# Kernel optimization log

Measured on AMD Instinct MI355X. Metric: run time of the kernel, lower is better.

## Reference

```python
import jax, jax.numpy as jnp
import numpy as np

N = 2048          # n_nodes
D = 512           # d_model
H = 8             # n_heads
DH = D // H       # head dim
FF = 4 * D
MAX_DIST = 10
LN_EPS = 1e-5


def setup_inputs() -> dict:
    key = jax.random.key(0)
    ks = jax.random.split(key, 20)
    s = 1.0 / np.sqrt(D)
    sf = 1.0 / np.sqrt(FF)
    return {
        "x": jax.random.normal(ks[0], (N, D), jnp.float32),
        "adj": (jax.random.uniform(ks[1], (N, N)) < 0.01).astype(jnp.float32),
        "spatial_emb": jax.random.normal(ks[2], (MAX_DIST + 1,), jnp.float32) * 0.02,
        "wq": jax.random.normal(ks[3], (D, D), jnp.float32) * s,
        "bq": jnp.zeros((D,), jnp.float32),
        "wk": jax.random.normal(ks[4], (D, D), jnp.float32) * s,
        "bk": jnp.zeros((D,), jnp.float32),
        "wv": jax.random.normal(ks[5], (D, D), jnp.float32) * s,
        "bv": jnp.zeros((D,), jnp.float32),
        "wo": jax.random.normal(ks[6], (D, D), jnp.float32) * s,
        "bo": jnp.zeros((D,), jnp.float32),
        "ln1_w": jnp.ones((D,), jnp.float32),
        "ln1_b": jnp.zeros((D,), jnp.float32),
        "w1": jax.random.normal(ks[7], (FF, D), jnp.float32) * s,
        "b1": jnp.zeros((FF,), jnp.float32),
        "w2": jax.random.normal(ks[8], (D, FF), jnp.float32) * sf,
        "b2": jnp.zeros((D,), jnp.float32),
        "ln2_w": jnp.ones((D,), jnp.float32),
        "ln2_b": jnp.zeros((D,), jnp.float32),
    }


def floyd_warshall(adj):
    # dist init: 1 where edge, inf otherwise, 0 on diagonal
    n = adj.shape[0]
    dist = jnp.where(adj > 0, 1.0, jnp.inf)
    dist = jnp.where(jnp.eye(n, dtype=bool), 0.0, dist)

    def body(k, dmat):
        row = jax.lax.dynamic_slice_in_dim(dmat, k, 1, axis=0)  # [1, n]
        col = jax.lax.dynamic_slice_in_dim(dmat, k, 1, axis=1)  # [n, 1]
        return jnp.minimum(dmat, col + row)

    dist = jax.lax.fori_loop(0, n, body, dist)
    return jnp.clip(dist, 0, MAX_DIST).astype(jnp.int32)  # [n, n]


def layer_norm(x, w, b):
    mu = jnp.mean(x, axis=-1, keepdims=True)
    var = jnp.mean(jnp.square(x - mu), axis=-1, keepdims=True)
    return (x - mu) * jax.lax.rsqrt(var + LN_EPS) * w + b


def reference(x, adj, spatial_emb, wq, bq, wk, bk, wv, bv, wo, bo,
              ln1_w, ln1_b, w1, b1, w2, b2, ln2_w, ln2_b):
    n = x.shape[0]
    sp_dist = floyd_warshall(adj)                       # [n, n] int32 in [0, 10]
    bias = spatial_emb[sp_dist]                         # [n, n] additive attn bias

    # multi-head attention with additive spatial bias (shared across heads)
    q = (x @ wq.T + bq).reshape(n, H, DH).transpose(1, 0, 2)  # [h, n, dh]
    k = (x @ wk.T + bk).reshape(n, H, DH).transpose(1, 0, 2)
    v = (x @ wv.T + bv).reshape(n, H, DH).transpose(1, 0, 2)
    scores = jnp.einsum('hnd,hmd->hnm', q, k) / np.sqrt(DH) + bias[None]
    attn = jax.nn.softmax(scores, axis=-1)
    ctx = jnp.einsum('hnm,hmd->hnd', attn, v)           # [h, n, dh]
    attn_out = ctx.transpose(1, 0, 2).reshape(n, D) @ wo.T + bo

    h = layer_norm(x + attn_out, ln1_w, ln1_b)
    ffn = jax.nn.gelu(h @ w1.T + b1, approximate=False) @ w2.T + b2
    return layer_norm(h + ffn, ln2_w, ln2_b)
```

## Files before the change

kernel.cpp:

```cpp
#include <hip/hip_runtime.h>
#include <cstdint>
#include <cstddef>


typedef __attribute__((ext_vector_type(8))) short short8;
typedef __attribute__((ext_vector_type(4))) float f32x4;

#define N_NODES 2048
#define DMODEL  512
#define NHEAD   8
#define DHEAD   64
#define FFDIM   2048

#define OFF_ADJB   (0)
#define OFF_DIST   (0x80000)
#define OFF_XB     (0x480000)
#define OFF_WQB    (0x680000)
#define OFF_WKB    (0x700000)
#define OFF_WVB    (0x780000)
#define OFF_WOB    (0x800000)
#define OFF_W1B    (0x880000)
#define OFF_W2B    (0xA80000)
#define OFF_QM     (0xC80000)
#define OFF_KM     (0xE80000)
#define OFF_VT     (0x1080000)
#define OFF_CTX    (0x1280000)
#define OFF_ATMP   (0x1480000)
#define OFF_H1     (0x1880000)
#define OFF_H1B    (0x1C80000)
#define OFF_MID    (0x1E80000)
#define OFF_FFN2   (0x2680000)

__device__ __forceinline__ unsigned short f2bf(float f) {
  union { float f; unsigned u; } c; c.f = f;
  unsigned r = c.u + 0x7FFFu + ((c.u >> 16) & 1u);
  return (unsigned short)(r >> 16);
}

__device__ __forceinline__ float bf2f(unsigned short u) {
  union { unsigned u; float f; } c; c.u = ((unsigned)u) << 16;
  return c.f;
}

__device__ __forceinline__ uint32_t cvtpk_bf16(float lo, float hi) {
  uint32_t r;
  asm("v_cvt_pk_bf16_f32 %0, %1, %2" : "=v"(r) : "v"(lo), "v"(hi));
  return r;
}

typedef const __attribute__((address_space(1))) unsigned int* as1_u32p;
typedef __attribute__((address_space(3))) unsigned int* as3_u32p;
__device__ __forceinline__ void gload_lds16(const void* g, void* l) {
  __builtin_amdgcn_global_load_lds((as1_u32p)g, (as3_u32p)l, 16, 0, 0);
}

__global__ void cvt_all_kernel(const float* __restrict__ x,
                               const float* __restrict__ wq, const float* __restrict__ wk,
                               const float* __restrict__ wv, const float* __restrict__ wo,
                               const float* __restrict__ w1, const float* __restrict__ w2,
                               unsigned short* __restrict__ xb,
                               unsigned short* __restrict__ wqb, unsigned short* __restrict__ wkb,
                               unsigned short* __restrict__ wvb, unsigned short* __restrict__ wob,
                               unsigned short* __restrict__ w1b, unsigned short* __restrict__ w2b) {
  int i = blockIdx.x * 256 + threadIdx.x;
  const float* src; unsigned short* dst; int off;
  if (i < 262144)      { src = x;  dst = xb;  off = i; }
  else if (i < 327680) { src = wq; dst = wqb; off = i - 262144; }
  else if (i < 393216) { src = wk; dst = wkb; off = i - 327680; }
  else if (i < 458752) { src = wv; dst = wvb; off = i - 393216; }
  else if (i < 524288) { src = wo; dst = wob; off = i - 458752; }
  else if (i < 786432) { src = w1; dst = w1b; off = i - 524288; }
  else                 { src = w2; dst = w2b; off = i - 786432; }
  float4 v = ((const float4*)src)[off];
  unsigned p0 = (unsigned)f2bf(v.x) | ((unsigned)f2bf(v.y) << 16);
  unsigned p1 = (unsigned)f2bf(v.z) | ((unsigned)f2bf(v.w) << 16);
  ((uint2*)dst)[off] = make_uint2(p0, p1);
}

__global__ void pack_adj_kernel(const float* __restrict__ adj, uint32_t* __restrict__ adjb) {
  int i = blockIdx.x;
  int tid = threadIdx.x, wid = tid >> 6, lane = tid & 63;
  for (int it = 0; it < 8; ++it) {
    int jbase = it * 256 + wid * 64;
    int j = jbase + lane;
    unsigned long long m = __ballot(adj[(size_t)i * 2048 + j] > 0.0f);
    int w32 = jbase >> 5;
    if (lane == 0)  adjb[i * 64 + w32]     = (uint32_t)m;
    if (lane == 32) adjb[i * 64 + w32 + 1] = (uint32_t)(m >> 32);
  }
}

__device__ __forceinline__ void bfs_body(int i, const uint32_t* __restrict__ adjb,
                                         uint8_t* __restrict__ dist, char* smem) {
  int tid = threadIdx.x, wid = tid >> 6, lane = tid & 63;

  uint4* comb_v = (uint4*)smem;
  uint32_t* wtot = (uint32_t*)(smem + 4096);
  uint16_t* list_s = (uint16_t*)(smem + 4112);
  const uint32_t* comb_u = (const uint32_t*)comb_v;

  uint32_t adjrow = adjb[i * 64 + lane];
  uint32_t diagm  = (lane == (i >> 5)) ? (1u << (i & 31)) : 0u;
  uint32_t front  = adjrow & ~diagm;
  uint32_t reach  = front | diagm;
  uint32_t dp0 = front;
  uint32_t dp1 = ~(front | diagm);
  uint32_t dp2 = 0u;
  uint32_t dp3 = dp1;

  for (int t = 2; t <= 9; ++t) {
    uint32_t fw = __shfl(front, wid * 16 + (lane >> 2));
    uint32_t fb = (fw >> ((lane & 3) * 8)) & 0xFFu;
    int cnt = __popc(fb);
    int scan = cnt;
    #pragma unroll
    for (int o = 1; o < 64; o <<= 1) {
      int u = __shfl_up(scan, o);
      if (lane >= o) scan += u;
    }
    if (lane == 63) wtot[wid] = (uint32_t)scan;
    __syncthreads();
    int w0 = (int)wtot[0], w1 = (int)wtot[1], w2 = (int)wtot[2], w3 = (int)wtot[3];
    int cnt_total = w0 + w1 + w2 + w3;
    if (cnt_total == 0) break;
    int base0 = (wid > 0 ? w0 : 0) + (wid > 1 ? w1 : 0) + (wid > 2 ? w2 : 0);
    int off = base0 + scan - cnt;
    int nodebase = tid * 8;
    while (fb) {
      int b = __builtin_ctz(fb);
      fb &= fb - 1u;
      list_s[off++] = (uint16_t)(nodebase + b);
    }
    int padded = (cnt_total + 63) & ~63;
    for (int k = cnt_total + tid; k < padded; k += 256)
      list_s[k] = (uint16_t)i;
    __syncthreads();

    uint4 acc = make_uint4(0u, 0u, 0u, 0u);
    int wsub = (lane & 15) * 4;
    for (int base = wid * 16; base < padded; base += 64) {
      #pragma unroll
      for (int j = 0; j < 4; ++j) {
        int node = list_s[base + j * 4 + (lane >> 4)];
        uint4 v = *(const uint4*)(adjb + node * 64 + wsub);
        acc.x |= v.x; acc.y |= v.y; acc.z |= v.z; acc.w |= v.w;
      }
    }
    comb_v[wid * 64 + lane] = acc;
    __syncthreads();
    uint32_t orv = 0;
    int idx = (lane >> 2) * 4 + (lane & 3);
    #pragma unroll
    for (int w4 = 0; w4 < 4; ++w4)
      #pragma unroll
      for (int g = 0; g < 4; ++g)
        orv |= comb_u[w4 * 256 + g * 64 + idx];
    uint32_t nreach = reach | orv;
    uint32_t nf = nreach & ~reach;
    dp0 = (dp0 & ~nf) | ((t & 1) ? nf : 0u);
    dp1 = (dp1 & ~nf) | ((t & 2) ? nf : 0u);
    dp2 = (dp2 & ~nf) | ((t & 4) ? nf : 0u);
    dp3 = (dp3 & ~nf) | ((t & 8) ? nf : 0u);
    front = nf;
    reach = nreach;
    __syncthreads();
  }

  uint32_t p0 = __shfl(dp0, wid * 16 + (lane >> 2));
  uint32_t p1 = __shfl(dp1, wid * 16 + (lane >> 2));
  uint32_t p2 = __shfl(dp2, wid * 16 + (lane >> 2));
  uint32_t p3 = __shfl(dp3, wid * 16 + (lane >> 2));
  int sh = (lane & 3) * 8;
  uint32_t lo = 0, hi = 0;
  #pragma unroll
  for (int j = 0; j < 4; ++j) {
    int bit = sh + j;
    uint32_t d = ((p0 >> bit) & 1u) | (((p1 >> bit) & 1u) << 1) |
                 (((p2 >> bit) & 1u) << 2) | (((p3 >> bit) & 1u) << 3);
    lo |= d << (8 * j);
  }
  #pragma unroll
  for (int j = 0; j < 4; ++j) {
    int bit = sh + 4 + j;
    uint32_t d = ((p0 >> bit) & 1u) | (((p1 >> bit) & 1u) << 1) |
                 (((p2 >> bit) & 1u) << 2) | (((p3 >> bit) & 1u) << 3);
    hi |= d << (8 * j);
  }
  ((uint2*)(dist + (size_t)i * 2048))[tid] = make_uint2(lo, hi);
}

__device__ __forceinline__ void gemm_core64(const short* __restrict__ A,
                                            const short* __restrict__ W,
                                            int K, int kstart, int kc,
                                            int am0, int bn0,
                                            f32x4 acc[2][2], char* smem) {
  int tid = threadIdx.x, wid = tid >> 6, lane = tid & 63;
  int c15 = lane & 15, g = lane >> 4;
  int wm = wid >> 1, wn = wid & 1;
  char* As = smem;
  char* Bs = smem + 8192;

  for (int kt = kstart; kt < kstart + kc; kt += 64) {
    __syncthreads();
    #pragma unroll
    for (int i = 0; i < 2; ++i) {
      int c   = i * 256 + tid;
      int row = c >> 3;
      int kg  = (c & 7) ^ (row & 7);
      gload_lds16(A + (size_t)(am0 + row) * K + kt + kg * 8,
                  As + i * 4096 + wid * 1024);
      gload_lds16(W + (size_t)(bn0 + row) * K + kt + kg * 8,
                  Bs + i * 4096 + wid * 1024);
    }
    __syncthreads();
    #pragma unroll
    for (int ks = 0; ks < 2; ++ks) {
      short8 af[2], bfr[2];
      #pragma unroll
      for (int mt = 0; mt < 2; ++mt) {
        int row   = wm * 32 + mt * 16 + c15;
        int chunk = (ks * 4 + g) ^ (row & 7);
        af[mt] = *(const short8*)(As + row * 128 + chunk * 16);
      }
      #pragma unroll
      for (int nt = 0; nt < 2; ++nt) {
        int row   = wn * 32 + nt * 16 + c15;
        int chunk = (ks * 4 + g) ^ (row & 7);
        bfr[nt] = *(const short8*)(Bs + row * 128 + chunk * 16);
      }
      #pragma unroll
      for (int mt = 0; mt < 2; ++mt)
        #pragma unroll
        for (int nt = 0; nt < 2; ++nt)
          acc[mt][nt] = __builtin_amdgcn_mfma_f32_16x16x32_bf16(af[mt], bfr[nt], acc[mt][nt], 0, 0, 0);
    }
  }
}

__device__ __forceinline__ void qkv_body(int bx, int by,
    const short* __restrict__ A,
    const short* __restrict__ W0, const short* __restrict__ W1, const short* __restrict__ W2,
    const float* __restrict__ b0, const float* __restrict__ b1, const float* __restrict__ b2,
    unsigned short* __restrict__ outq, unsigned short* __restrict__ outk,
    unsigned short* __restrict__ outv, char* smem) {
  int region = by >> 3;
  const short* W    = (region == 0) ? W0 : (region == 1) ? W1 : W2;
  const float* bias = (region == 0) ? b0 : (region == 1) ? b1 : b2;
  int bn0 = (by & 7) * 64;
  int am0 = bx * 64;

  f32x4 acc[2][2] = {};
  gemm_core64(A, W, 512, 0, 512, am0, bn0, acc, smem);

  int tid = threadIdx.x, wid = tid >> 6, lane = tid & 63;
  int c15 = lane & 15, g = lane >> 4;
  int wm = wid >> 1, wn = wid & 1;

  #pragma unroll
  for (int mt = 0; mt < 2; ++mt)
    #pragma unroll
    for (int nt = 0; nt < 2; ++nt)
      #pragma unroll
      for (int r = 0; r < 4; ++r) {
        int row = am0 + wm * 32 + mt * 16 + g * 4 + r;
        int col = bn0 + wn * 32 + nt * 16 + c15;
        float v = acc[mt][nt][r] + bias[col];
        if (region == 0)      outq[(size_t)row * 512 + col] = f2bf(v);
        else if (region == 1) outk[(size_t)row * 512 + col] = f2bf(v);
        else                  outv[(size_t)col * 2048 + row] = f2bf(v);
      }
}

__global__ __launch_bounds__(256) void bfs_qkv_kernel(
    const uint32_t* __restrict__ adjb, uint8_t* __restrict__ dist,
    const short* __restrict__ xb,
    const short* __restrict__ wqb, const short* __restrict__ wkb, const short* __restrict__ wvb,
    const float* __restrict__ bq, const float* __restrict__ bk, const float* __restrict__ bv,
    unsigned short* __restrict__ qm, unsigned short* __restrict__ km,
    unsigned short* __restrict__ vT) {
  __shared__ __align__(16) char smem[16384];
  int b = blockIdx.x;
  if (b < 2048) {
    bfs_body(b, adjb, dist, smem);
  } else {
    int gidx = b - 2048;
    qkv_body(gidx & 31, gidx >> 5, xb, wqb, wkb, wvb, bq, bk, bv, qm, km, vT, smem);
  }
}

template <int MODE>
__global__ __launch_bounds__(256) void gemm_kernel(
    const short* __restrict__ A,
    const short* __restrict__ W0,
    const float* __restrict__ b0,
    float* __restrict__ of0, float* __restrict__ of1,
    float* __restrict__ of2, float* __restrict__ of3,
    unsigned short* __restrict__ outb,
    int K, int kc, int ldo) {
  __shared__ __align__(16) char smem[16384];
  int by = blockIdx.y, z = blockIdx.z;
  int bn0 = by * 64;
  int am0 = blockIdx.x * 64;

  f32x4 acc[2][2] = {};
  gemm_core64(A, W0, K, z * kc, kc, am0, bn0, acc, smem);

  int tid = threadIdx.x, wid = tid >> 6, lane = tid & 63;
  int c15 = lane & 15, g = lane >> 4;
  int wm = wid >> 1, wn = wid & 1;
  float* of = (z == 0) ? of0 : (z == 1) ? of1 : (z == 2) ? of2 : of3;

  #pragma unroll
  for (int mt = 0; mt < 2; ++mt)
    #pragma unroll
    for (int nt = 0; nt < 2; ++nt)
      #pragma unroll
      for (int r = 0; r < 4; ++r) {
        int row = am0 + wm * 32 + mt * 16 + g * 4 + r;
        int col = bn0 + wn * 32 + nt * 16 + c15;
        if (MODE == 1) {
          float v = acc[mt][nt][r] + ((z == 0) ? b0[col] : 0.0f);
          of[(size_t)row * ldo + col] = v;
        } else {
          float v = acc[mt][nt][r] + b0[col];
          float gv = 0.5f * v * (1.0f + erff(v * 0.70710678118654752f));
          outb[(size_t)row * ldo + col] = f2bf(gv);
        }
      }
}

__global__ __launch_bounds__(256, 4) void attn_kernel(
    const short* __restrict__ qm, const short* __restrict__ km,
    const short* __restrict__ vT, const uint8_t* __restrict__ dist,
    const float* __restrict__ semb, unsigned short* __restrict__ po,
    float* __restrict__ pml) {
  int qt = blockIdx.x, h = blockIdx.y, z = blockIdx.z;
  int tid = threadIdx.x, wid = tid >> 6, lane = tid & 63;
  int c15 = lane & 15, g = lane >> 4;

  __shared__ __align__(16) char Ks[8192];
  __shared__ __align__(16) char Vs[8192];
  __shared__ __align__(16) uint8_t Ds[4096];
  __shared__ float semb_s[12];
  if (tid < 11) semb_s[tid] = semb[tid];

  int q0  = qt * 64;
  int wq0 = q0 + wid * 16;
  int kvz = z * 512;

  short8 aq[2];
  #pragma unroll
  for (int ks = 0; ks < 2; ++ks)
    aq[ks] = *(const short8*)(qm + (size_t)(wq0 + c15) * 512 + h * 64 + ks * 32 + g * 8);

  int i  = tid;
  int r0 = i >> 3,        c0 = (i & 7) ^ (r0 & 7);
  int r1 = (256 + i) >> 3, c1 = ((256 + i) & 7) ^ (r1 & 7);
  int dr = i >> 2,        dc = (i & 3) ^ (dr & 3);

  f32x4 o[4] = {};
  float m = -1e30f, l = 0.0f;

  for (int t = 0; t < 8; ++t) {
    int kv0 = kvz + t * 64;

    __syncthreads();
    gload_lds16(km + (size_t)(kv0 + r0) * 512 + h * 64 + c0 * 8, Ks + wid * 1024);
    gload_lds16(km + (size_t)(kv0 + r1) * 512 + h * 64 + c1 * 8, Ks + 4096 + wid * 1024);
    gload_lds16(vT + (size_t)(h * 64 + r0) * 2048 + kv0 + c0 * 8, Vs + wid * 1024);
    gload_lds16(vT + (size_t)(h * 64 + r1) * 2048 + kv0 + c1 * 8, Vs + 4096 + wid * 1024);
    gload_lds16(dist + (size_t)(q0 + dr) * 2048 + kv0 + dc * 16, Ds + wid * 1024);
    __syncthreads();

    f32x4 sacc[4] = {};
    __builtin_amdgcn_s_setprio(1);
    #pragma unroll
    for (int nt = 0; nt < 4; ++nt) {
      int row = nt * 16 + c15;
      #pragma unroll
      for (int ks = 0; ks < 2; ++ks) {
        short8 bk = *(const short8*)(Ks + row * 128 + (((ks * 4 + g) ^ (row & 7)) * 16));
        sacc[nt] = __builtin_amdgcn_mfma_f32_16x16x32_bf16(bk, aq[ks], sacc[nt], 0, 0, 0);
      }
    }
    __builtin_amdgcn_s_setprio(0);

    int drow = wid * 16 + c15;
    float rmax = -1e30f;
    #pragma unroll
    for (int nt = 0; nt < 4; ++nt) {
      uint32_t d32 = *(const uint32_t*)(Ds + drow * 64 + ((nt ^ (drow & 3)) * 16) + g * 4);
      #pragma unroll
      for (int r = 0; r < 4; ++r) {
        float s = sacc[nt][r] * 0.125f + semb_s[(d32 >> (8 * r)) & 0xFFu];
        sacc[nt][r] = s;
        rmax = fmaxf(rmax, s);
      }
    }
    rmax = fmaxf(rmax, __shfl_xor(rmax, 16));
    rmax = fmaxf(rmax, __shfl_xor(rmax, 32));

    float mn = fmaxf(m, rmax);
    float pscale = __expf(m - mn);
    m = mn;
    float rsum = 0.0f;
    #pragma unroll
    for (int nt = 0; nt < 4; ++nt)
      #pragma unroll
      for (int r = 0; r < 4; ++r) {
        float p = __expf(sacc[nt][r] - m);
        sacc[nt][r] = p;
        rsum += p;
      }
    rsum += __shfl_xor(rsum, 16);
    rsum += __shfl_xor(rsum, 32);
    l = l * pscale + rsum;

    float psr[4];
    #pragma unroll
    for (int r = 0; r < 4; ++r) psr[r] = __shfl(pscale, g * 4 + r);
    #pragma unroll
    for (int dt = 0; dt < 4; ++dt)
      #pragma unroll
      for (int r = 0; r < 4; ++r)
        o[dt][r] *= psr[r];

    int src_lo = c15 + (g & 1) * 32;
    int src_hi = src_lo + 16;
    int sel = g >> 1;
    short8 pa[2];
    {
      uint32_t p00 = cvtpk_bf16(sacc[0][0], sacc[0][1]);
      uint32_t p01 = cvtpk_bf16(sacc[0][2], sacc[0][3]);
      uint32_t p10 = cvtpk_bf16(sacc[1][0], sacc[1][1]);
      uint32_t p11 = cvtpk_bf16(sacc[1][2], sacc[1][3]);
      uint32_t a0 = (uint32_t)__shfl((int)p00, src_lo);
      uint32_t a1 = (uint32_t)__shfl((int)p01, src_lo);
      uint32_t a2 = (uint32_t)__shfl((int)p00, src_hi);
      uint32_t a3 = (uint32_t)__shfl((int)p01, src_hi);
      uint32_t b0 = (uint32_t)__shfl((int)p10, src_lo);
      uint32_t b1 = (uint32_t)__shfl((int)p11, src_lo);
      uint32_t b2 = (uint32_t)__shfl((int)p10, src_hi);
      uint32_t b3 = (uint32_t)__shfl((int)p11, src_hi);
      union { short8 s8; uint32_t u[4]; } up;
      up.u[0] = sel ? b0 : a0;
      up.u[1] = sel ? b1 : a1;
      up.u[2] = sel ? b2 : a2;
      up.u[3] = sel ? b3 : a3;
      pa[0] = up.s8;
    }
    {
      uint32_t p00 = cvtpk_bf16(sacc[2][0], sacc[2][1]);
      uint32_t p01 = cvtpk_bf16(sacc[2][2], sacc[2][3]);
      uint32_t p10 = cvtpk_bf16(sacc[3][0], sacc[3][1]);
      uint32_t p11 = cvtpk_bf16(sacc[3][2], sacc[3][3]);
      uint32_t a0 = (uint32_t)__shfl((int)p00, src_lo);
      uint32_t a1 = (uint32_t)__shfl((int)p01, src_lo);
      uint32_t a2 = (uint32_t)__shfl((int)p00, src_hi);
      uint32_t a3 = (uint32_t)__shfl((int)p01, src_hi);
      uint32_t b0 = (uint32_t)__shfl((int)p10, src_lo);
      uint32_t b1 = (uint32_t)__shfl((int)p11, src_lo);
      uint32_t b2 = (uint32_t)__shfl((int)p10, src_hi);
      uint32_t b3 = (uint32_t)__shfl((int)p11, src_hi);
      union { short8 s8; uint32_t u[4]; } up;
      up.u[0] = sel ? b0 : a0;
      up.u[1] = sel ? b1 : a1;
      up.u[2] = sel ? b2 : a2;
      up.u[3] = sel ? b3 : a3;
      pa[1] = up.s8;
    }

    __builtin_amdgcn_s_setprio(1);
    #pragma unroll
    for (int dt = 0; dt < 4; ++dt) {
      int row = dt * 16 + c15;
      #pragma unroll
      for (int ks = 0; ks < 2; ++ks) {
        short8 bv = *(const short8*)(Vs + row * 128 + (((ks * 4 + g) ^ (row & 7)) * 16));
        o[dt] = __builtin_amdgcn_mfma_f32_16x16x32_bf16(pa[ks], bv, o[dt], 0, 0, 0);
      }
    }
    __builtin_amdgcn_s_setprio(0);
  }

  #pragma unroll
  for (int dt = 0; dt < 4; ++dt)
    #pragma unroll
    for (int r = 0; r < 4; ++r) {
      int q = wq0 + g * 4 + r;
      po[((size_t)z * 2048 + q) * 512 + h * 64 + dt * 16 + c15] = f2bf(o[dt][r]);
    }
  if (g == 0) {
    int q = wq0 + c15;
    pml[(((size_t)z * 2048 + q) * 8 + h) * 2]     = m;
    pml[(((size_t)z * 2048 + q) * 8 + h) * 2 + 1] = l;
  }
}

__global__ __launch_bounds__(256) void attn_combine_kernel(
    const unsigned short* __restrict__ po, const float* __restrict__ pml,
    unsigned short* __restrict__ ctx) {
  int q = blockIdx.x, tid = threadIdx.x;
  #pragma unroll
  for (int half = 0; half < 2; ++half) {
    int d = half * 256 + tid;
    int h = d >> 6;
    float mm[4], ll[4];
    float ms = -1e30f;
    #pragma unroll
    for (int zz = 0; zz < 4; ++zz) {
      mm[zz] = pml[(((size_t)zz * 2048 + q) * 8 + h) * 2];
      ll[zz] = pml[(((size_t)zz * 2048 + q) * 8 + h) * 2 + 1];
      ms = fmaxf(ms, mm[zz]);
    }
    float num = 0.0f, den = 0.0f;
    #pragma unroll
    for (int zz = 0; zz < 4; ++zz) {
      float e = __expf(mm[zz] - ms);
      num += bf2f(po[((size_t)zz * 2048 + q) * 512 + d]) * e;
      den += ll[zz] * e;
    }
    ctx[(size_t)q * 512 + d] = f2bf(num / den);
  }
}

template <int NP, bool WB>
__global__ __launch_bounds__(256) void ln_kernel(
    const float* __restrict__ a,
    const float* __restrict__ p0, const float* __restrict__ p1,
    const float* __restrict__ p2, const float* __restrict__ p3,
    const float* __restrict__ w, const float* __restrict__ bb,
    float* __restrict__ out, unsigned short* __restrict__ outb) {
  int row = blockIdx.x, tid = threadIdx.x;
  size_t base = (size_t)row * 512;
  float v0 = a[base + tid]       + p0[base + tid];
  float v1 = a[base + tid + 256] + p0[base + tid + 256];
  if (NP > 1) { v0 += p1[base + tid]; v1 += p1[base + tid + 256]; }
  if (NP > 2) { v0 += p2[base + tid]; v1 += p2[base + tid + 256]; }
  if (NP > 3) { v0 += p3[base + tid]; v1 += p3[base + tid + 256]; }
  float s = v0 + v1, q = v0 * v0 + v1 * v1;
  for (int o = 32; o > 0; o >>= 1) { s += __shfl_down(s, o); q += __shfl_down(q, o); }
  __shared__ float rs[4], rq[4], bc[2];
  int wid = tid >> 6, lane = tid & 63;
  if (lane == 0) { rs[wid] = s; rq[wid] = q; }
  __syncthreads();
  if (tid == 0) {
    float S = rs[0] + rs[1] + rs[2] + rs[3];
    float Q = rq[0] + rq[1] + rq[2] + rq[3];
    float mu = S * (1.0f / 512.0f);
    bc[0] = mu;
    bc[1] = Q * (1.0f / 512.0f) - mu * mu;
  }
  __syncthreads();
  float mu = bc[0], inv = rsqrtf(bc[1] + 1e-5f);
  float o0 = (v0 - mu) * inv * w[tid] + bb[tid];
  float o1 = (v1 - mu) * inv * w[tid + 256] + bb[tid + 256];
  out[base + tid] = o0;
  out[base + tid + 256] = o1;
  if (WB) {
    outb[base + tid] = f2bf(o0);
    outb[base + tid + 256] = f2bf(o1);
  }
}

extern "C" void kernel_launch(void* const* d_in, const int* in_sizes, int n_in,
                              void* d_out, int out_size, void* d_ws, size_t ws_size,
                              hipStream_t stream) {
  (void)in_sizes; (void)n_in; (void)out_size; (void)ws_size;
  const float* x    = (const float*)d_in[0];
  const float* adj  = (const float*)d_in[1];
  const float* semb = (const float*)d_in[2];
  const float* wq   = (const float*)d_in[3];
  const float* bq   = (const float*)d_in[4];
  const float* wk   = (const float*)d_in[5];
  const float* bk   = (const float*)d_in[6];
  const float* wv   = (const float*)d_in[7];
  const float* bv   = (const float*)d_in[8];
  const float* wo   = (const float*)d_in[9];
  const float* bo   = (const float*)d_in[10];
  const float* ln1w = (const float*)d_in[11];
  const float* ln1b = (const float*)d_in[12];
  const float* w1   = (const float*)d_in[13];
  const float* b1   = (const float*)d_in[14];
  const float* w2   = (const float*)d_in[15];
  const float* b2   = (const float*)d_in[16];
  const float* ln2w = (const float*)d_in[17];
  const float* ln2b = (const float*)d_in[18];
  float* out = (float*)d_out;
  char* ws = (char*)d_ws;

  uint32_t*       adjb = (uint32_t*)(ws + OFF_ADJB);
  uint8_t*        dist = (uint8_t*)(ws + OFF_DIST);
  unsigned short* xb   = (unsigned short*)(ws + OFF_XB);
  unsigned short* wqb  = (unsigned short*)(ws + OFF_WQB);
  unsigned short* wkb  = (unsigned short*)(ws + OFF_WKB);
  unsigned short* wvb  = (unsigned short*)(ws + OFF_WVB);
  unsigned short* wob  = (unsigned short*)(ws + OFF_WOB);
  unsigned short* w1b  = (unsigned short*)(ws + OFF_W1B);
  unsigned short* w2b  = (unsigned short*)(ws + OFF_W2B);
  unsigned short* qm   = (unsigned short*)(ws + OFF_QM);
  unsigned short* km   = (unsigned short*)(ws + OFF_KM);
  unsigned short* vT   = (unsigned short*)(ws + OFF_VT);
  unsigned short* ctx  = (unsigned short*)(ws + OFF_CTX);
  float*          atmp = (float*)(ws + OFF_ATMP);
  float*          h1   = (float*)(ws + OFF_H1);
  unsigned short* h1b  = (unsigned short*)(ws + OFF_H1B);
  unsigned short* mid  = (unsigned short*)(ws + OFF_MID);
  float*          ffn2 = (float*)(ws + OFF_FFN2);
  unsigned short* po   = (unsigned short*)(ws + OFF_MID);
  float* pml   = (float*)(ws + OFF_FFN2);
  float* distf = (float*)(ws + OFF_DIST);
  float* qmf   = (float*)(ws + OFF_QM);
  float* vtf   = (float*)(ws + OFF_VT);

  cvt_all_kernel<<<4096, 256, 0, stream>>>(x, wq, wk, wv, wo, w1, w2,
                                           xb, wqb, wkb, wvb, wob, w1b, w2b);

  pack_adj_kernel<<<2048, 256, 0, stream>>>(adj, adjb);

  bfs_qkv_kernel<<<2816, 256, 0, stream>>>(
      adjb, dist, (const short*)xb,
      (const short*)wqb, (const short*)wkb, (const short*)wvb,
      bq, bk, bv, qm, km, vT);

  attn_kernel<<<dim3(32, 8, 4), 256, 0, stream>>>(
      (const short*)qm, (const short*)km, (const short*)vT, dist, semb, po, pml);
  attn_combine_kernel<<<2048, 256, 0, stream>>>(po, pml, ctx);

  gemm_kernel<1><<<dim3(32, 8, 2), 256, 0, stream>>>(
      (const short*)ctx, (const short*)wob, bo,
      atmp, distf, nullptr, nullptr, nullptr, 512, 256, 512);

  ln_kernel<2, true><<<2048, 256, 0, stream>>>(x, atmp, distf, nullptr, nullptr,
                                               ln1w, ln1b, h1, h1b);

  gemm_kernel<2><<<dim3(32, 32), 256, 0, stream>>>(
      (const short*)h1b, (const short*)w1b, b1,
      nullptr, nullptr, nullptr, nullptr, mid, 512, 512, 2048);

  gemm_kernel<1><<<dim3(32, 8, 4), 256, 0, stream>>>(
      (const short*)mid, (const short*)w2b, b2,
      ffn2, distf, qmf, vtf, nullptr, 2048, 512, 512);

  ln_kernel<4, false><<<2048, 256, 0, stream>>>(h1, ffn2, distf, qmf, vtf,
                                                ln2w, ln2b, out, nullptr);
}
```

Measured before the change: 142.0 us.

## Add direction-optimizing bottom-up BFS with transposed adjacency bitmap

Adds a transposed bit-packed adjacency and switches the per-source BFS to a bottom-up step once the unvisited set is smaller than half the frontier. In that step each unvisited node checks its incoming edges against the frontier, instead of the frontier OR-ing the rows of all its neighbours. This is meant to cut the gather traffic on late BFS levels of the dense random graph. It also splits the fused BFS+QKV launch into separate kernels and adds an extra transpose-pack kernel, which removes the overlap between the two and adds launch and pack cost.

```diff
diff --git a/kernel.cpp b/kernel.cpp
--- a/kernel.cpp
+++ b/kernel.cpp
@@ -90,13 +90,28 @@
   }
 }
 
-__device__ __forceinline__ void bfs_body(int i, const uint32_t* __restrict__ adjb,
-                                         uint8_t* __restrict__ dist, char* smem) {
+__global__ __launch_bounds__(256) void pack_adjT_kernel(const float* __restrict__ adj,
+                                                        uint32_t* __restrict__ adjbT) {
+  int iw = blockIdx.x;
+  int j  = blockIdx.y * 256 + threadIdx.x;
+  uint32_t acc = 0;
+  #pragma unroll
+  for (int r = 0; r < 32; ++r)
+    acc |= (adj[(size_t)(iw * 32 + r) * 2048 + j] > 0.0f ? 1u : 0u) << r;
+  adjbT[(size_t)j * 64 + iw] = acc;
+}
+
+__global__ __launch_bounds__(256) void bfs_kernel(const uint32_t* __restrict__ adjb,
+                                                  const uint32_t* __restrict__ adjbT,
+                                                  uint8_t* __restrict__ dist) {
+  int i = blockIdx.x;
   int tid = threadIdx.x, wid = tid >> 6, lane = tid & 63;
 
-  uint4* comb_v = (uint4*)smem;
-  uint32_t* wtot = (uint32_t*)(smem + 4096);
-  uint16_t* list_s = (uint16_t*)(smem + 4112);
+  __shared__ uint16_t list_s[2112];
+  __shared__ uint4 comb_v[4][64];
+  __shared__ uint32_t wtot[4];
+  __shared__ uint32_t fl_s[64];
+  __shared__ uint32_t nf_s[64];
   const uint32_t* comb_u = (const uint32_t*)comb_v;
 
   uint32_t adjrow = adjb[i * 64 + lane];
@@ -109,60 +124,113 @@
   uint32_t dp3 = dp1;
 
   for (int t = 2; t <= 9; ++t) {
-    uint32_t fw = __shfl(front, wid * 16 + (lane >> 2));
-    uint32_t fb = (fw >> ((lane & 3) * 8)) & 0xFFu;
-    int cnt = __popc(fb);
-    int scan = cnt;
-    #pragma unroll
-    for (int o = 1; o < 64; o <<= 1) {
-      int u = __shfl_up(scan, o);
-      if (lane >= o) scan += u;
-    }
-    if (lane == 63) wtot[wid] = (uint32_t)scan;
-    __syncthreads();
-    int w0 = (int)wtot[0], w1 = (int)wtot[1], w2 = (int)wtot[2], w3 = (int)wtot[3];
-    int cnt_total = w0 + w1 + w2 + w3;
-    if (cnt_total == 0) break;
-    int base0 = (wid > 0 ? w0 : 0) + (wid > 1 ? w1 : 0) + (wid > 2 ? w2 : 0);
-    int off = base0 + scan - cnt;
-    int nodebase = tid * 8;
-    while (fb) {
-      int b = __builtin_ctz(fb);
-      fb &= fb - 1u;
-      list_s[off++] = (uint16_t)(nodebase + b);
-    }
-    int padded = (cnt_total + 63) & ~63;
-    for (int k = cnt_total + tid; k < padded; k += 256)
-      list_s[k] = (uint16_t)i;
-    __syncthreads();
-
-    uint4 acc = make_uint4(0u, 0u, 0u, 0u);
-    int wsub = (lane & 15) * 4;
-    for (int base = wid * 16; base < padded; base += 64) {
-      #pragma unroll
-      for (int j = 0; j < 4; ++j) {
-        int node = list_s[base + j * 4 + (lane >> 4)];
-        uint4 v = *(const uint4*)(adjb + node * 64 + wsub);
-        acc.x |= v.x; acc.y |= v.y; acc.z |= v.z; acc.w |= v.w;
-      }
-    }
-    comb_v[wid * 64 + lane] = acc;
-    __syncthreads();
-    uint32_t orv = 0;
-    int idx = (lane >> 2) * 4 + (lane & 3);
-    #pragma unroll
-    for (int w4 = 0; w4 < 4; ++w4)
-      #pragma unroll
-      for (int g = 0; g < 4; ++g)
-        orv |= comb_u[w4 * 256 + g * 64 + idx];
-    uint32_t nreach = reach | orv;
-    uint32_t nf = nreach & ~reach;
+    int cf = __popc(front), cu = __popc(~reach);
+    #pragma unroll
+    for (int o = 1; o < 64; o <<= 1) { cf += __shfl_xor(cf, o); cu += __shfl_xor(cu, o); }
+    if (cf == 0) break;
+    bool bottom_up = (cu < (cf >> 1));
+
+    uint32_t nf;
+    if (!bottom_up) {
+      uint32_t fw = __shfl(front, wid * 16 + (lane >> 2));
+      uint32_t fb = (fw >> ((lane & 3) * 8)) & 0xFFu;
+      int cnt = __popc(fb);
+      int scan = cnt;
+      #pragma unroll
+      for (int o = 1; o < 64; o <<= 1) {
+        int u = __shfl_up(scan, o);
+        if (lane >= o) scan += u;
+      }
+      if (lane == 63) wtot[wid] = (uint32_t)scan;
+      __syncthreads();
+      int w0 = (int)wtot[0], w1 = (int)wtot[1], w2 = (int)wtot[2], w3 = (int)wtot[3];
+      int cnt_total = w0 + w1 + w2 + w3;
+      int base0 = (wid > 0 ? w0 : 0) + (wid > 1 ? w1 : 0) + (wid > 2 ? w2 : 0);
+      int off = base0 + scan - cnt;
+      int nodebase = tid * 8;
+      while (fb) {
+        int b = __builtin_ctz(fb);
+        fb &= fb - 1u;
+        list_s[off++] = (uint16_t)(nodebase + b);
+      }
+      int padded = (cnt_total + 63) & ~63;
+      for (int k = cnt_total + tid; k < padded; k += 256)
+        list_s[k] = (uint16_t)i;
+      __syncthreads();
+
+      uint4 acc = make_uint4(0u, 0u, 0u, 0u);
+      int wsub = (lane & 15) * 4;
+      for (int base = wid * 16; base < padded; base += 64) {
+        #pragma unroll
+        for (int j = 0; j < 4; ++j) {
+          int node = list_s[base + j * 4 + (lane >> 4)];
+          uint4 v = *(const uint4*)(adjb + node * 64 + wsub);
+          acc.x |= v.x; acc.y |= v.y; acc.z |= v.z; acc.w |= v.w;
+        }
+      }
+      comb_v[wid][lane] = acc;
+      __syncthreads();
+      uint32_t orv = 0;
+      int idx = (lane >> 2) * 4 + (lane & 3);
+      #pragma unroll
+      for (int w4 = 0; w4 < 4; ++w4)
+        #pragma unroll
+        for (int g = 0; g < 4; ++g)
+          orv |= comb_u[w4 * 256 + g * 64 + idx];
+      nf = orv & ~reach;
+    } else {
+      uint32_t uv = ~reach;
+      uint32_t fw = __shfl(uv, wid * 16 + (lane >> 2));
+      uint32_t fb = (fw >> ((lane & 3) * 8)) & 0xFFu;
+      int cnt = __popc(fb);
+      int scan = cnt;
+      #pragma unroll
+      for (int o = 1; o < 64; o <<= 1) {
+        int u = __shfl_up(scan, o);
+        if (lane >= o) scan += u;
+      }
+      if (lane == 63) wtot[wid] = (uint32_t)scan;
+      if (wid == 0) { fl_s[lane] = front; nf_s[lane] = 0u; }
+      __syncthreads();
+      int w0 = (int)wtot[0], w1 = (int)wtot[1], w2 = (int)wtot[2], w3 = (int)wtot[3];
+      int cnt_total = w0 + w1 + w2 + w3;
+      int base0 = (wid > 0 ? w0 : 0) + (wid > 1 ? w1 : 0) + (wid > 2 ? w2 : 0);
+      int off = base0 + scan - cnt;
+      int nodebase = tid * 8;
+      while (fb) {
+        int b = __builtin_ctz(fb);
+        fb &= fb - 1u;
+        list_s[off++] = (uint16_t)(nodebase + b);
+      }
+      int padded = (cnt_total + 63) & ~63;
+      for (int k = cnt_total + tid; k < padded; k += 256)
+        list_s[k] = (uint16_t)i;
+      __syncthreads();
+
+      int wsub = (lane & 15) * 4;
+      unsigned long long gm = 0xFFFFull << ((lane >> 4) * 16);
+      for (int base = wid * 16; base < padded; base += 64) {
+        #pragma unroll
+        for (int j = 0; j < 4; ++j) {
+          int node = list_s[base + j * 4 + (lane >> 4)];
+          uint4 v = *(const uint4*)(adjbT + node * 64 + wsub);
+          uint32_t loc = (v.x & fl_s[wsub]) | (v.y & fl_s[wsub + 1]) |
+                         (v.z & fl_s[wsub + 2]) | (v.w & fl_s[wsub + 3]);
+          unsigned long long b = __ballot(loc != 0u);
+          if (((lane & 15) == 0) && (b & gm))
+            atomicOr(&nf_s[node >> 5], 1u << (node & 31));
+        }
+      }
+      __syncthreads();
+      nf = nf_s[lane] & ~reach;
+    }
+
     dp0 = (dp0 & ~nf) | ((t & 1) ? nf : 0u);
     dp1 = (dp1 & ~nf) | ((t & 2) ? nf : 0u);
     dp2 = (dp2 & ~nf) | ((t & 4) ? nf : 0u);
     dp3 = (dp3 & ~nf) | ((t & 8) ? nf : 0u);
     front = nf;
-    reach = nreach;
+    reach |= nf;
     __syncthreads();
   }
 
@@ -237,17 +305,19 @@
   }
 }
 
-__device__ __forceinline__ void qkv_body(int bx, int by,
+__global__ __launch_bounds__(256) void qkv_kernel(
     const short* __restrict__ A,
     const short* __restrict__ W0, const short* __restrict__ W1, const short* __restrict__ W2,
     const float* __restrict__ b0, const float* __restrict__ b1, const float* __restrict__ b2,
     unsigned short* __restrict__ outq, unsigned short* __restrict__ outk,
-    unsigned short* __restrict__ outv, char* smem) {
+    unsigned short* __restrict__ outv) {
+  __shared__ __align__(16) char smem[16384];
+  int by = blockIdx.y;
   int region = by >> 3;
   const short* W    = (region == 0) ? W0 : (region == 1) ? W1 : W2;
   const float* bias = (region == 0) ? b0 : (region == 1) ? b1 : b2;
   int bn0 = (by & 7) * 64;
-  int am0 = bx * 64;
+  int am0 = blockIdx.x * 64;
 
   f32x4 acc[2][2] = {};
   gemm_core64(A, W, 512, 0, 512, am0, bn0, acc, smem);
@@ -269,23 +339,6 @@
         else if (region == 1) outk[(size_t)row * 512 + col] = f2bf(v);
         else                  outv[(size_t)col * 2048 + row] = f2bf(v);
       }
-}
-
-__global__ __launch_bounds__(256) void bfs_qkv_kernel(
-    const uint32_t* __restrict__ adjb, uint8_t* __restrict__ dist,
-    const short* __restrict__ xb,
-    const short* __restrict__ wqb, const short* __restrict__ wkb, const short* __restrict__ wvb,
-    const float* __restrict__ bq, const float* __restrict__ bk, const float* __restrict__ bv,
-    unsigned short* __restrict__ qm, unsigned short* __restrict__ km,
-    unsigned short* __restrict__ vT) {
-  __shared__ __align__(16) char smem[16384];
-  int b = blockIdx.x;
-  if (b < 2048) {
-    bfs_body(b, adjb, dist, smem);
-  } else {
-    int gidx = b - 2048;
-    qkv_body(gidx & 31, gidx >> 5, xb, wqb, wkb, wvb, bq, bk, bv, qm, km, vT, smem);
-  }
 }
 
 template <int MODE>
@@ -607,6 +660,7 @@
   unsigned short* h1b  = (unsigned short*)(ws + OFF_H1B);
   unsigned short* mid  = (unsigned short*)(ws + OFF_MID);
   float*          ffn2 = (float*)(ws + OFF_FFN2);
+  uint32_t* adjbT = (uint32_t*)(ws + OFF_MID);
   unsigned short* po   = (unsigned short*)(ws + OFF_MID);
   float* pml   = (float*)(ws + OFF_FFN2);
   float* distf = (float*)(ws + OFF_DIST);
@@ -617,10 +671,12 @@
                                            xb, wqb, wkb, wvb, wob, w1b, w2b);
 
   pack_adj_kernel<<<2048, 256, 0, stream>>>(adj, adjb);
-
-  bfs_qkv_kernel<<<2816, 256, 0, stream>>>(
-      adjb, dist, (const short*)xb,
-      (const short*)wqb, (const short*)wkb, (const short*)wvb,
+  pack_adjT_kernel<<<dim3(64, 8), 256, 0, stream>>>(adj, adjbT);
+
+  bfs_kernel<<<2048, 256, 0, stream>>>(adjb, adjbT, dist);
+
+  qkv_kernel<<<dim3(32, 24), 256, 0, stream>>>(
+      (const short*)xb, (const short*)wqb, (const short*)wkb, (const short*)wvb,
       bq, bk, bv, qm, km, vT);
 
   attn_kernel<<<dim3(32, 8, 4), 256, 0, stream>>>(
```

After: 131.2 us, median of 2. 1.08x faster.
